# Performance work log

Measured on AMD Instinct MI355X. Metric: run time of the kernel, lower is better.

The kernel has to match this reference:

```python
import jax, jax.numpy as jnp
import numpy as np

EPS = 1e-6
KH = KW = 3  # square kernel the 5-point plus stencil unpacks into


def setup_inputs() -> dict:
    key = jax.random.key(0)
    k1, k2, k3 = jax.random.split(key, 3)
    bs, ci, co, H, W = 8, 256, 256, 128, 128
    x = jax.random.normal(k1, (bs, ci, H, W), dtype=jnp.float32)
    y = jax.random.normal(k2, (bs, ci), dtype=jnp.float32)
    # packed stencil weights (channels_out, channels_in, stencil_size)
    weights = jax.random.normal(k3, (co, ci, 5), dtype=jnp.float32) * 0.02
    # flat indices into the 3x3 kernel for stencil pts (0,1),(1,0),(1,1),(1,2),(2,1)
    stencil_index = jnp.array([1, 3, 4, 5, 7], dtype=jnp.int32)
    return {"x": x, "y": y, "weights": weights, "stencil_index": stencil_index}


def _modulated_lattice_conv(x, y, weights, stencil_index):
    bs, ci, H, W = x.shape
    co = weights.shape[0]
    # StyleGAN2-style modulation: w2 * (w1 + 1)  -> [bs, co, ci, S]
    w = weights[None, :, :, :] * (y[:, None, :, None] + 1.0)
    # demodulation: rsqrt of sum over (in, stencil) dims
    d = jax.lax.rsqrt(jnp.sum(w * w, axis=(2, 3), keepdims=True) + EPS)
    w = w * d
    # fold batch into output channels for groups=batch trick
    w = w.reshape(bs * co, ci, -1)
    # unpack non-square stencil into zero-padded square kernel (irregular scatter)
    full = jnp.zeros((bs * co, ci, KH * KW), dtype=w.dtype)
    full = full.at[:, :, stencil_index].set(w)
    kern = full.reshape(bs * co, ci, KH, KW)
    # grouped conv: input reshaped to (1, bs*ci, H, W), feature_group_count=bs
    out = jax.lax.conv_general_dilated(
        x.reshape(1, bs * ci, H, W), kern,
        window_strides=(1, 1), padding='SAME',
        feature_group_count=bs,
        dimension_numbers=('NCHW', 'OIHW', 'NCHW'))
    return out.reshape(bs, co, H, W)


def reference(x, y, weights, stencil_index):
    return _modulated_lattice_conv(x, y, weights, stencil_index)
```

## Files before the change

kernel.cpp:

```cpp
#include <hip/hip_runtime.h>


typedef short v8s __attribute__((ext_vector_type(8)));
typedef float v4f __attribute__((ext_vector_type(4)));
typedef int   v4i __attribute__((ext_vector_type(4)));

#define BS 8
#define CI 256
#define CO 256
#define HH 128
#define WW 128

#define WF_CK 10240
#define RSTR_B 5632
#define RSTR_I 1408
#define XBUF_I (6 * RSTR_I)
#define XBUF_B (6 * RSTR_B)

#define GLOAD_LDS16(g, l)                                                  \
    __builtin_amdgcn_global_load_lds(                                      \
        (__attribute__((address_space(1))) void*)(g),                      \
        (__attribute__((address_space(3))) void*)(l), 16, 0, 0)

__device__ __forceinline__ unsigned short f2bf(float f) {
    unsigned u = __builtin_bit_cast(unsigned, f);
    u += 0x7FFFu + ((u >> 16) & 1u);
    return (unsigned short)(u >> 16);
}

__global__ __launch_bounds__(256) void prep_kernel(const float* __restrict__ x,
                                                   const float* __restrict__ y,
                                                   const float* __restrict__ wgt,
                                                   short* __restrict__ wfrag,
                                                   unsigned int* __restrict__ xt) {
    __shared__ float tr[32 * 132];
    __shared__ float red[4];

    if (blockIdx.x < 2048) {
        const int bo = blockIdx.x;
        const int b = bo >> 8, o = bo & 255;
        const int ci = threadIdx.x;
        const float ym = y[b * CI + ci] + 1.0f;
        const float* wp = wgt + (o * CI + ci) * 5;
        float w[5];
        float s2 = 0.f;
        #pragma unroll
        for (int s = 0; s < 5; ++s) { w[s] = wp[s]; s2 += w[s] * w[s]; }
        float ss = ym * ym * s2;
        #pragma unroll
        for (int off = 32; off > 0; off >>= 1) ss += __shfl_down(ss, off);
        if ((threadIdx.x & 63) == 0) red[threadIdx.x >> 6] = ss;
        __syncthreads();
        const float tot = red[0] + red[1] + red[2] + red[3];
        const float scale = ym * rsqrtf(tot + 1e-6f);
        const int ot = o >> 6, mt = (o >> 4) & 3, m = o & 15;
        const int ck = ci >> 5, quad = (ci >> 3) & 3, j = ci & 7;
        size_t base = ((size_t)(b * 4 + ot) * 8 + ck) * WF_CK + quad * 128 + m * 8 + j;
        #pragma unroll
        for (int s = 0; s < 5; ++s)
            wfrag[base + (size_t)(s * 4 + mt) * 512] = (short)f2bf(w[s] * scale);
    } else {
        const int bid = blockIdx.x - 2048;
        const int b  = bid >> 10;
        const int ck = (bid >> 7) & 7;
        const int h  = bid & 127;
        const int tid = threadIdx.x;
        #pragma unroll
        for (int i = 0; i < 4; ++i) {
            int q  = tid + i * 256;
            int c  = q >> 5;
            int qp = q & 31;
            v4f v = *(const v4f*)&x[((size_t)(b * CI + ck * 32 + c) * HH + h) * WW
                                    + qp * 4];
            *(v4f*)&tr[c * 132 + qp * 4] = v;
        }
        __syncthreads();
        const int px = tid >> 1, half = tid & 1;
        unsigned pk[8];
        #pragma unroll
        for (int k = 0; k < 8; ++k) {
            float f0 = tr[(half * 16 + 2 * k)     * 132 + px];
            float f1 = tr[(half * 16 + 2 * k + 1) * 132 + px];
            pk[k] = (unsigned)f2bf(f0) | ((unsigned)f2bf(f1) << 16);
        }
        unsigned int* dst = xt + ((size_t)((b * 8 + ck) * 16384 + h * 128 + px)) * 16
                               + half * 8;
        *(v4i*)dst       = (v4i){(int)pk[0], (int)pk[1], (int)pk[2], (int)pk[3]};
        *(v4i*)(dst + 4) = (v4i){(int)pk[4], (int)pk[5], (int)pk[6], (int)pk[7]};
    }
}

__global__ __launch_bounds__(256) void wprep2_kernel(const float* __restrict__ y,
                                                     const float* __restrict__ wgt,
                                                     short* __restrict__ wfrag) {
    const int bo = blockIdx.x;
    const int b = bo >> 8, o = bo & 255;
    const int ci = threadIdx.x;
    const float ym = y[b * CI + ci] + 1.0f;
    const float* wp = wgt + (o * CI + ci) * 5;
    float w[5];
    float s2 = 0.f;
    #pragma unroll
    for (int s = 0; s < 5; ++s) { w[s] = wp[s]; s2 += w[s] * w[s]; }
    float ss = ym * ym * s2;
    #pragma unroll
    for (int off = 32; off > 0; off >>= 1) ss += __shfl_down(ss, off);
    __shared__ float red[4];
    if ((threadIdx.x & 63) == 0) red[threadIdx.x >> 6] = ss;
    __syncthreads();
    const float tot = red[0] + red[1] + red[2] + red[3];
    const float scale = ym * rsqrtf(tot + 1e-6f);
    const int ot = o >> 6, mt = (o >> 4) & 3, m = o & 15;
    const int ck = ci >> 5, quad = (ci >> 3) & 3, j = ci & 7;
    size_t base = ((size_t)(b * 4 + ot) * 8 + ck) * WF_CK + quad * 128 + m * 8 + j;
    #pragma unroll
    for (int s = 0; s < 5; ++s)
        wfrag[base + (size_t)(s * 4 + mt) * 512] = (short)f2bf(w[s] * scale);
}

__global__ __launch_bounds__(256, 2) void conv3_kernel(const char* __restrict__ xt,
                                                       const short* __restrict__ wfrag,
                                                       float* __restrict__ out) {
    const int b     = blockIdx.z;
    const int ot    = blockIdx.y;
    const int oBase = ot * 64;
    const int st    = blockIdx.x;
    const int r0    = (st >> 1) * 4;
    const int c0    = (st & 1) * 64;
    const bool left = (c0 == 0);

    const int tid  = threadIdx.x;
    const int wid  = tid >> 6;
    const int lane = tid & 63;
    const int l15  = lane & 15;
    const int quad = lane >> 4;

    __shared__ __align__(16) int xs[2 * XBUF_I];

    v4f acc[4][4];
    #pragma unroll
    for (int a = 0; a < 4; ++a)
        #pragma unroll
        for (int n = 0; n < 4; ++n) acc[a][n] = (v4f){0.f, 0.f, 0.f, 0.f};

    const v4i z4 = (v4i){0, 0, 0, 0};
    #pragma unroll
    for (int bb = 0; bb < 2; ++bb) {
        int* xb = xs + bb * XBUF_I;
        if (r0 == 0)
            for (int i = tid; i < 264; i += 256) *(v4i*)&xb[i * 4] = z4;
        if (r0 == HH - 4)
            for (int i = tid; i < 264; i += 256) *(v4i*)&xb[5 * RSTR_I + i * 4] = z4;
        if (left && tid < 24) *(v4i*)&xb[(tid >> 2) * RSTR_I + (tid & 3) * 4] = z4;
    }

    const int row = r0 + wid;
    const short* wfb = wfrag + (size_t)(b * 4 + ot) * 8 * WF_CK;
    const bool rz = (!left) && (l15 == 15);
    const int gstartB = left ? 0 : (c0 - 1) * 64;
    const int lshift  = left ? 64 : 0;

    auto stage = [&](int ckk, int bufsel) {
        const char* planep = xt + (((size_t)(b * 8 + ckk)) << 20);
        char* lbase = (char*)xs + bufsel * XBUF_B;
        #pragma unroll
        for (int rsel = 0; rsel < 2; ++rsel) {
            int rr = wid + rsel * 4;
            if (rr < 6) {
                bool skip = (r0 == 0 && rr == 0) || (r0 == HH - 4 && rr == 5);
                if (!skip) {
                    int gr = r0 - 1 + rr;
                    const char* gb = planep + (size_t)gr * 8192 + gstartB + lane * 16;
                    char* lb = lbase + rr * RSTR_B + lshift;
                    #pragma unroll
                    for (int t = 0; t < 5; ++t)
                        GLOAD_LDS16(gb + t * 1024, lb + t * 1024);
                }
            }
        }
    };

    stage(0, 0);
    __syncthreads();

    const int dh[5] = {-1, 0, 0, 0, 1};
    const int dw[5] = { 0,-1, 0, 1, 0};

    #pragma unroll 2
    for (int ck = 0; ck < 8; ++ck) {
        const short* wfc = wfb + (size_t)ck * WF_CK;
        const int* xb = xs + (ck & 1) * XBUF_I;

        v8s af[20];
        #pragma unroll
        for (int sm = 0; sm < 20; ++sm)
            af[sm] = *(const v8s*)(wfc + (size_t)(sm * 4 + quad) * 128 + l15 * 8);
        __builtin_amdgcn_sched_barrier(0);

        if (ck < 7) stage(ck + 1, (ck + 1) & 1);

        #pragma unroll
        for (int s = 0; s < 5; ++s) {
            const int xrow = wid + 1 + dh[s];
            const int xc0  = 1 + dw[s];
            #pragma unroll
            for (int nt = 0; nt < 4; ++nt) {
                v4i bi = *(const v4i*)&xb[xrow * RSTR_I + (nt * 16 + l15 + xc0) * 16
                                          + quad * 4];
                if (s == 3 && nt == 3) { if (rz) bi = z4; }
                v8s bfr = __builtin_bit_cast(v8s, bi);
                #pragma unroll
                for (int mt = 0; mt < 4; ++mt)
                    acc[mt][nt] = __builtin_amdgcn_mfma_f32_16x16x32_bf16(
                        af[s * 4 + mt], bfr, acc[mt][nt], 0, 0, 0);
            }
        }
        __syncthreads();
    }

    #pragma unroll
    for (int mt = 0; mt < 4; ++mt)
        #pragma unroll
        for (int nt = 0; nt < 4; ++nt)
            #pragma unroll
            for (int r = 0; r < 4; ++r) {
                int o = oBase + mt * 16 + quad * 4 + r;
                int c = c0 + nt * 16 + l15;
                out[((size_t)(b * CO + o) * HH + row) * WW + c] = acc[mt][nt][r];
            }
}

__global__ __launch_bounds__(256, 4) void conv_kernel(const float* __restrict__ x,
                                                      const short* __restrict__ wfrag,
                                                      float* __restrict__ out) {
    const int b     = blockIdx.z;
    const int ot    = blockIdx.y;
    const int oBase = ot * 64;
    const int st    = blockIdx.x;
    const int r0    = (st >> 1) * 4;
    const int c0    = (st & 1) * 64;
    const int tid  = threadIdx.x;
    const int wid  = tid >> 6;
    const int lane = tid & 63;
    const int l15  = lane & 15;
    const int quad = lane >> 4;
    #define PXS 20
    __shared__ __align__(16) int xs[6 * 66 * PXS];
    v4f acc[4][4];
    #pragma unroll
    for (int a = 0; a < 4; ++a)
        #pragma unroll
        for (int n = 0; n < 4; ++n) acc[a][n] = (v4f){0.f, 0.f, 0.f, 0.f};
    const int row = r0 + wid;
    const short* wfb = wfrag + (size_t)(b * 4 + ot) * 8 * WF_CK;
    const int dh[5] = {-1, 0, 0, 0, 1};
    const int dw[5] = { 0,-1, 0, 1, 0};
    for (int ck = 0; ck < 8; ++ck) {
        const int ic0 = ck * 32;
        #pragma unroll
        for (int t = 0; t < 6; ++t) {
            int idx = tid + t * 256;
            int cp  = idx & 15;
            int tmp = idx >> 4;
            int cq  = tmp & 15;
            int rr  = tmp >> 4;
            int gr  = r0 - 1 + rr;
            v4f a0 = (v4f){0.f, 0.f, 0.f, 0.f}, a1 = a0;
            if (gr >= 0 && gr < HH) {
                const float* xp = x + ((size_t)(b * CI + ic0 + cp * 2) * HH + gr) * WW
                                    + (c0 + cq * 4);
                a0 = *(const v4f*)xp;
                a1 = *(const v4f*)(xp + HH * WW);
            }
            int base = (rr * 66 + cq * 4 + 1) * PXS + cp;
            #pragma unroll
            for (int k = 0; k < 4; ++k)
                xs[base + k * PXS] =
                    (int)((unsigned)f2bf(a0[k]) | ((unsigned)f2bf(a1[k]) << 16));
        }
        if (tid < 192) {
            int cp   = tid & 15;
            int tmp  = tid >> 4;
            int side = (tmp >= 6) ? 1 : 0;
            int rr   = tmp - 6 * side;
            int gr   = r0 - 1 + rr;
            int gc   = side ? (c0 + 64) : (c0 - 1);
            float v0 = 0.f, v1 = 0.f;
            if (gr >= 0 && gr < HH && gc >= 0 && gc < WW) {
                const float* xp = x + ((size_t)(b * CI + ic0 + cp * 2) * HH + gr) * WW + gc;
                v0 = xp[0];
                v1 = xp[HH * WW];
            }
            int col = side ? 65 : 0;
            xs[(rr * 66 + col) * PXS + cp] =
                (int)((unsigned)f2bf(v0) | ((unsigned)f2bf(v1) << 16));
        }
        __syncthreads();
        const short* wfc = wfb + (size_t)ck * WF_CK;
        #pragma unroll
        for (int s = 0; s < 5; ++s) {
            const int xrow = wid + 1 + dh[s];
            const int xc0  = 1 + dw[s];
            v8s af[4];
            #pragma unroll
            for (int mt = 0; mt < 4; ++mt)
                af[mt] = *(const v8s*)(wfc + (size_t)((s * 4 + mt) * 4 + quad) * 128
                                           + l15 * 8);
            #pragma unroll
            for (int nt = 0; nt < 4; ++nt) {
                int px = xrow * 66 + nt * 16 + l15 + xc0;
                v4i bi = *(const v4i*)&xs[px * PXS + quad * 4];
                v8s bfr = __builtin_bit_cast(v8s, bi);
                #pragma unroll
                for (int mt = 0; mt < 4; ++mt)
                    acc[mt][nt] = __builtin_amdgcn_mfma_f32_16x16x32_bf16(
                        af[mt], bfr, acc[mt][nt], 0, 0, 0);
            }
        }
        __syncthreads();
    }
    #pragma unroll
    for (int mt = 0; mt < 4; ++mt)
        #pragma unroll
        for (int nt = 0; nt < 4; ++nt)
            #pragma unroll
            for (int r = 0; r < 4; ++r) {
                int o = oBase + mt * 16 + quad * 4 + r;
                int c = c0 + nt * 16 + l15;
                out[((size_t)(b * CO + o) * HH + row) * WW + c] = acc[mt][nt][r];
            }
}

__global__ __launch_bounds__(256) void demod_kernel(const float* __restrict__ y,
                                                    const float* __restrict__ wgt,
                                                    float* __restrict__ dbuf) {
    const int bo = blockIdx.x;
    const int b = bo >> 8, o = bo & 255;
    const int i = threadIdx.x;
    const float* wp = wgt + (o * CI + i) * 5;
    const float ym = y[b * CI + i] + 1.0f;
    float s2 = 0.f;
    #pragma unroll
    for (int s = 0; s < 5; ++s) { float w = wp[s]; s2 += w * w; }
    float val = ym * ym * s2;
    #pragma unroll
    for (int off = 32; off > 0; off >>= 1) val += __shfl_down(val, off);
    __shared__ float red[4];
    if ((threadIdx.x & 63) == 0) red[threadIdx.x >> 6] = val;
    __syncthreads();
    if (threadIdx.x == 0) dbuf[bo] = rsqrtf(red[0] + red[1] + red[2] + red[3] + 1e-6f);
}

__global__ __launch_bounds__(256) void conv_kernel_fb(const float* __restrict__ x,
                                                      const float* __restrict__ y,
                                                      const float* __restrict__ wgt,
                                                      const float* __restrict__ dbuf,
                                                      float* __restrict__ out) {
    const int b     = blockIdx.z;
    const int oBase = blockIdx.y * 64;
    const int st    = blockIdx.x;
    const int r0    = (st >> 1) * 4;
    const int c0    = (st & 1) * 64;
    const int tid  = threadIdx.x;
    const int wid  = tid >> 6;
    const int lane = tid & 63;
    const int l15  = lane & 15;
    const int quad = lane >> 4;
    __shared__ int   xs4[16 * 412];
    __shared__ short wlds[5 * 4 * 4 * 16 * 8];
    v4f acc[4][4];
    #pragma unroll
    for (int a = 0; a < 4; ++a)
        #pragma unroll
        for (int n = 0; n < 4; ++n) acc[a][n] = (v4f){0.f, 0.f, 0.f, 0.f};
    const int row = r0 + wid;
    for (int ic0 = 0; ic0 < CI; ic0 += 32) {
        for (int t = 0; t < 25; ++t) {
            int idx = tid + t * 256;
            if (idx < 6336) {
                int cp  = idx / 396;
                int rem = idx - cp * 396;
                int rr  = rem / 66;
                int cc  = rem - rr * 66;
                int gr  = r0 - 1 + rr;
                int gc  = c0 - 1 + cc;
                float v0 = 0.f, v1 = 0.f;
                if (gr >= 0 && gr < HH && gc >= 0 && gc < WW) {
                    const float* xp = x + ((size_t)(b * CI + ic0 + cp * 2) * HH + gr) * WW + gc;
                    v0 = xp[0];
                    v1 = xp[HH * WW];
                }
                xs4[cp * 412 + rr * 68 + cc] =
                    (int)((unsigned)f2bf(v0) | ((unsigned)f2bf(v1) << 16));
            }
        }
        #pragma unroll
        for (int p = 0; p < 8; ++p) {
            int pidx = tid + p * 256;
            int ol = pidx >> 5;
            int il = pidx & 31;
            int o  = oBase + ol;
            int ci = ic0 + il;
            float scale = (y[b * CI + ci] + 1.0f) * dbuf[b * CO + o];
            const float* wp = wgt + (o * CI + ci) * 5;
            int base = (((ol >> 4) * 4 + (il >> 3)) * 16 + (ol & 15)) * 8 + (il & 7);
            #pragma unroll
            for (int s = 0; s < 5; ++s)
                wlds[base + s * (4 * 4 * 16 * 8)] = (short)f2bf(wp[s] * scale);
        }
        __syncthreads();
        const int dh[5] = {-1, 0, 0, 0, 1};
        const int dw[5] = { 0,-1, 0, 1, 0};
        #pragma unroll
        for (int s = 0; s < 5; ++s) {
            int xrow = wid + 1 + dh[s];
            int xcb  = l15 + 1 + dw[s];
            v8s af[4];
            #pragma unroll
            for (int mt = 0; mt < 4; ++mt)
                af[mt] = *(const v8s*)&wlds[(((s * 4 + mt) * 4 + quad) * 16 + l15) * 8];
            #pragma unroll
            for (int nt = 0; nt < 4; ++nt) {
                v4i bi;
                #pragma unroll
                for (int p = 0; p < 4; ++p)
                    bi[p] = xs4[(quad * 4 + p) * 412 + xrow * 68 + nt * 16 + xcb];
                v8s bfr = __builtin_bit_cast(v8s, bi);
                #pragma unroll
                for (int mt = 0; mt < 4; ++mt)
                    acc[mt][nt] = __builtin_amdgcn_mfma_f32_16x16x32_bf16(
                        af[mt], bfr, acc[mt][nt], 0, 0, 0);
            }
        }
        __syncthreads();
    }
    #pragma unroll
    for (int mt = 0; mt < 4; ++mt)
        #pragma unroll
        for (int nt = 0; nt < 4; ++nt)
            #pragma unroll
            for (int r = 0; r < 4; ++r) {
                int o = oBase + mt * 16 + quad * 4 + r;
                int c = c0 + nt * 16 + l15;
                out[((size_t)(b * CO + o) * HH + row) * WW + c] = acc[mt][nt][r];
            }
}

extern "C" void kernel_launch(void* const* d_in, const int* in_sizes, int n_in,
                              void* d_out, int out_size, void* d_ws, size_t ws_size,
                              hipStream_t stream) {
    const float* x   = (const float*)d_in[0];
    const float* y   = (const float*)d_in[1];
    const float* wgt = (const float*)d_in[2];
    float* out = (float*)d_out;

    const size_t WF_BYTES = (size_t)BS * 4 * 8 * WF_CK * sizeof(short);
    const size_t XT_OFF   = WF_BYTES + 8192;
    const size_t XT_BYTES = (size_t)BS * 8 * 16384 * 64;
    const size_t NEED_FULL = XT_OFF + XT_BYTES + 1024;
    const size_t NEED_MID  = WF_BYTES + 8192;

    short* wfrag = (short*)d_ws;

    if (ws_size >= NEED_FULL) {
        unsigned int* xt = (unsigned int*)((char*)d_ws + XT_OFF);
        prep_kernel<<<dim3(2048 + BS * 8 * HH), dim3(256), 0, stream>>>(
            x, y, wgt, wfrag, xt);
        conv3_kernel<<<dim3(64, CO / 64, BS), dim3(256), 0, stream>>>(
            (const char*)xt, wfrag, out);
    } else if (ws_size >= NEED_MID) {
        wprep2_kernel<<<dim3(BS * CO), dim3(256), 0, stream>>>(y, wgt, wfrag);
        conv_kernel<<<dim3(64, CO / 64, BS), dim3(256), 0, stream>>>(x, wfrag, out);
    } else {
        float* dbuf = (float*)d_ws;
        demod_kernel<<<dim3(BS * CO), dim3(256), 0, stream>>>(y, wgt, dbuf);
        conv_kernel_fb<<<dim3(64, CO / 64, BS), dim3(256), 0, stream>>>(x, y, wgt, dbuf, out);
    }
}
```

Baseline: 312.3 us.

## Double rows per conv block and drop LDS double-buffering in conv3 kernel

Each conv3 block now covers 8 output rows instead of 4, so each wave computes two rows and reuses each weight fragment load across both rows. Halo rows are loaded 10 per 8 instead of 6 per 4, and the grid halves. The double-buffered prefetch is replaced by a single buffer with load-then-sync, which removes the overlap of global loads with MFMA work. Accumulators double to 128 floats per lane, which raises register pressure and may lower occupancy.

```diff
diff --git a/kernel.cpp b/kernel.cpp
--- a/kernel.cpp
+++ b/kernel.cpp
@@ -14,8 +14,6 @@
 #define WF_CK 10240
 #define RSTR_B 5632
 #define RSTR_I 1408
-#define XBUF_I (6 * RSTR_I)
-#define XBUF_B (6 * RSTR_B)
 
 #define GLOAD_LDS16(g, l)                                                  \
     __builtin_amdgcn_global_load_lds(                                      \
@@ -125,7 +123,7 @@
     const int ot    = blockIdx.y;
     const int oBase = ot * 64;
     const int st    = blockIdx.x;
-    const int r0    = (st >> 1) * 4;
+    const int r0    = (st >> 1) * 8;
     const int c0    = (st & 1) * 64;
     const bool left = (c0 == 0);
 
@@ -135,99 +133,92 @@
     const int l15  = lane & 15;
     const int quad = lane >> 4;
 
-    __shared__ __align__(16) int xs[2 * XBUF_I];
-
-    v4f acc[4][4];
-    #pragma unroll
-    for (int a = 0; a < 4; ++a)
-        #pragma unroll
-        for (int n = 0; n < 4; ++n) acc[a][n] = (v4f){0.f, 0.f, 0.f, 0.f};
+    __shared__ __align__(16) int xs[10 * RSTR_I];
+
+    v4f acc[2][4][4];
+    #pragma unroll
+    for (int r = 0; r < 2; ++r)
+        #pragma unroll
+        for (int a = 0; a < 4; ++a)
+            #pragma unroll
+            for (int n = 0; n < 4; ++n) acc[r][a][n] = (v4f){0.f, 0.f, 0.f, 0.f};
 
     const v4i z4 = (v4i){0, 0, 0, 0};
-    #pragma unroll
-    for (int bb = 0; bb < 2; ++bb) {
-        int* xb = xs + bb * XBUF_I;
-        if (r0 == 0)
-            for (int i = tid; i < 264; i += 256) *(v4i*)&xb[i * 4] = z4;
-        if (r0 == HH - 4)
-            for (int i = tid; i < 264; i += 256) *(v4i*)&xb[5 * RSTR_I + i * 4] = z4;
-        if (left && tid < 24) *(v4i*)&xb[(tid >> 2) * RSTR_I + (tid & 3) * 4] = z4;
-    }
-
-    const int row = r0 + wid;
+    if (r0 == 0)
+        for (int i = tid; i < 264; i += 256) *(v4i*)&xs[i * 4] = z4;
+    if (r0 == HH - 8)
+        for (int i = tid; i < 264; i += 256) *(v4i*)&xs[9 * RSTR_I + i * 4] = z4;
+    if (left && tid < 40) *(v4i*)&xs[(tid >> 2) * RSTR_I + (tid & 3) * 4] = z4;
+
     const short* wfb = wfrag + (size_t)(b * 4 + ot) * 8 * WF_CK;
     const bool rz = (!left) && (l15 == 15);
     const int gstartB = left ? 0 : (c0 - 1) * 64;
     const int lshift  = left ? 64 : 0;
 
-    auto stage = [&](int ckk, int bufsel) {
-        const char* planep = xt + (((size_t)(b * 8 + ckk)) << 20);
-        char* lbase = (char*)xs + bufsel * XBUF_B;
-        #pragma unroll
-        for (int rsel = 0; rsel < 2; ++rsel) {
+    const int dh[5] = {-1, 0, 0, 0, 1};
+    const int dw[5] = { 0,-1, 0, 1, 0};
+
+    for (int ck = 0; ck < 8; ++ck) {
+        const char* planep = xt + (((size_t)(b * 8 + ck)) << 20);
+        #pragma unroll
+        for (int rsel = 0; rsel < 3; ++rsel) {
             int rr = wid + rsel * 4;
-            if (rr < 6) {
-                bool skip = (r0 == 0 && rr == 0) || (r0 == HH - 4 && rr == 5);
+            if (rr < 10) {
+                bool skip = (r0 == 0 && rr == 0) || (r0 == HH - 8 && rr == 9);
                 if (!skip) {
                     int gr = r0 - 1 + rr;
                     const char* gb = planep + (size_t)gr * 8192 + gstartB + lane * 16;
-                    char* lb = lbase + rr * RSTR_B + lshift;
+                    char* lb = (char*)xs + rr * RSTR_B + lshift;
                     #pragma unroll
                     for (int t = 0; t < 5; ++t)
                         GLOAD_LDS16(gb + t * 1024, lb + t * 1024);
                 }
             }
         }
-    };
-
-    stage(0, 0);
-    __syncthreads();
-
-    const int dh[5] = {-1, 0, 0, 0, 1};
-    const int dw[5] = { 0,-1, 0, 1, 0};
-
-    #pragma unroll 2
-    for (int ck = 0; ck < 8; ++ck) {
+        __syncthreads();
+
         const short* wfc = wfb + (size_t)ck * WF_CK;
-        const int* xb = xs + (ck & 1) * XBUF_I;
-
-        v8s af[20];
-        #pragma unroll
-        for (int sm = 0; sm < 20; ++sm)
-            af[sm] = *(const v8s*)(wfc + (size_t)(sm * 4 + quad) * 128 + l15 * 8);
-        __builtin_amdgcn_sched_barrier(0);
-
-        if (ck < 7) stage(ck + 1, (ck + 1) & 1);
-
         #pragma unroll
         for (int s = 0; s < 5; ++s) {
-            const int xrow = wid + 1 + dh[s];
-            const int xc0  = 1 + dw[s];
-            #pragma unroll
-            for (int nt = 0; nt < 4; ++nt) {
-                v4i bi = *(const v4i*)&xb[xrow * RSTR_I + (nt * 16 + l15 + xc0) * 16
-                                          + quad * 4];
-                if (s == 3 && nt == 3) { if (rz) bi = z4; }
-                v8s bfr = __builtin_bit_cast(v8s, bi);
+            const int xc0 = 1 + dw[s];
+            v8s af[4];
+            #pragma unroll
+            for (int mt = 0; mt < 4; ++mt)
+                af[mt] = *(const v8s*)(wfc + (size_t)((s * 4 + mt) * 4 + quad) * 128
+                                           + l15 * 8);
+            #pragma unroll
+            for (int r = 0; r < 2; ++r) {
+                const int xrow = 2 * wid + r + 1 + dh[s];
                 #pragma unroll
-                for (int mt = 0; mt < 4; ++mt)
-                    acc[mt][nt] = __builtin_amdgcn_mfma_f32_16x16x32_bf16(
-                        af[s * 4 + mt], bfr, acc[mt][nt], 0, 0, 0);
-            }
-        }
-        __syncthreads();
-    }
-
-    #pragma unroll
-    for (int mt = 0; mt < 4; ++mt)
-        #pragma unroll
-        for (int nt = 0; nt < 4; ++nt)
-            #pragma unroll
-            for (int r = 0; r < 4; ++r) {
-                int o = oBase + mt * 16 + quad * 4 + r;
-                int c = c0 + nt * 16 + l15;
-                out[((size_t)(b * CO + o) * HH + row) * WW + c] = acc[mt][nt][r];
-            }
+                for (int nt = 0; nt < 4; ++nt) {
+                    v4i bi = *(const v4i*)&xs[xrow * RSTR_I
+                                              + (nt * 16 + l15 + xc0) * 16 + quad * 4];
+                    if (s == 3 && nt == 3) { if (rz) bi = z4; }
+                    v8s bfr = __builtin_bit_cast(v8s, bi);
+                    #pragma unroll
+                    for (int mt = 0; mt < 4; ++mt)
+                        acc[r][mt][nt] = __builtin_amdgcn_mfma_f32_16x16x32_bf16(
+                            af[mt], bfr, acc[r][mt][nt], 0, 0, 0);
+                }
+            }
+        }
+        __syncthreads();
+    }
+
+    #pragma unroll
+    for (int r = 0; r < 2; ++r) {
+        const int row = r0 + 2 * wid + r;
+        #pragma unroll
+        for (int mt = 0; mt < 4; ++mt)
+            #pragma unroll
+            for (int nt = 0; nt < 4; ++nt)
+                #pragma unroll
+                for (int rg = 0; rg < 4; ++rg) {
+                    int o = oBase + mt * 16 + quad * 4 + rg;
+                    int c = c0 + nt * 16 + l15;
+                    out[((size_t)(b * CO + o) * HH + row) * WW + c] = acc[r][mt][nt][rg];
+                }
+    }
 }
 
 __global__ __launch_bounds__(256, 4) void conv_kernel(const float* __restrict__ x,
@@ -466,7 +457,7 @@
         unsigned int* xt = (unsigned int*)((char*)d_ws + XT_OFF);
         prep_kernel<<<dim3(2048 + BS * 8 * HH), dim3(256), 0, stream>>>(
             x, y, wgt, wfrag, xt);
-        conv3_kernel<<<dim3(64, CO / 64, BS), dim3(256), 0, stream>>>(
+        conv3_kernel<<<dim3(32, CO / 64, BS), dim3(256), 0, stream>>>(
             (const char*)xt, wfrag, out);
     } else if (ws_size >= NEED_MID) {
         wprep2_kernel<<<dim3(BS * CO), dim3(256), 0, stream>>>(y, wgt, wfrag);
```

Result: no change. 314.0 us (+0.5%).

## Swizzle LDS tile layout and pipeline staging with explicit vmcnt waits

Applied to the files above, without the earlier changes.

Rewrites the input staging so every wave issues a uniform eight global-to-LDS loads, with row indices clamped instead of skipped. Boundary zero-padding moves out of LDS pre-zeroing and into register masks at MFMA operand load time. An XOR swizzle is applied to the LDS layout to reduce bank conflicts, and the read offsets are precomputed. Per-iteration __syncthreads is replaced by manual s_waitcnt vmcnt counters plus s_barrier, so weight loads and next-chunk staging overlap with compute. The hand-counted vmcnt values are fragile: they depend on exact load counts, and a miscount could cause a race.

```diff
diff --git a/kernel.cpp b/kernel.cpp
--- a/kernel.cpp
+++ b/kernel.cpp
@@ -143,71 +143,73 @@
         #pragma unroll
         for (int n = 0; n < 4; ++n) acc[a][n] = (v4f){0.f, 0.f, 0.f, 0.f};
 
-    const v4i z4 = (v4i){0, 0, 0, 0};
-    #pragma unroll
-    for (int bb = 0; bb < 2; ++bb) {
-        int* xb = xs + bb * XBUF_I;
-        if (r0 == 0)
-            for (int i = tid; i < 264; i += 256) *(v4i*)&xb[i * 4] = z4;
-        if (r0 == HH - 4)
-            for (int i = tid; i < 264; i += 256) *(v4i*)&xb[5 * RSTR_I + i * 4] = z4;
-        if (left && tid < 24) *(v4i*)&xb[(tid >> 2) * RSTR_I + (tid & 3) * 4] = z4;
-    }
-
     const int row = r0 + wid;
     const short* wfb = wfrag + (size_t)(b * 4 + ot) * 8 * WF_CK;
-    const bool rz = (!left) && (l15 == 15);
-    const int gstartB = left ? 0 : (c0 - 1) * 64;
-    const int lshift  = left ? 64 : 0;
+    const int gstartB = (c0 - 1) * 64;
+
+    const bool rzm  = (!left) && (l15 == 15);
+    const bool lzm  = left && (l15 == 0);
+    const bool topz = (r0 == 0)      && (wid == 0);
+    const bool botz = (r0 == HH - 4) && (wid == 3);
+    const v4i z4 = (v4i){0, 0, 0, 0};
+
+    const int dh[5] = {-1, 0, 0, 0, 1};
+    const int dw[5] = { 0,-1, 0, 1, 0};
+
+    int goff[8], loff[8];
+    #pragma unroll
+    for (int k = 0; k < 8; ++k) {
+        int q  = wid + 4 * k;
+        int qq = q < 30 ? q : q - 2;
+        int rr = qq / 5, t = qq - rr * 5;
+        int gr = r0 - 1 + rr;
+        gr = gr < 0 ? 0 : (gr > 127 ? 127 : gr);
+        int l  = t * 64 + lane;
+        int gx = l ^ ((l >> 3) & 7);
+        goff[k] = gr * 8192 + gstartB + gx * 16;
+        loff[k] = rr * RSTR_B + l * 16;
+    }
+
+    int boff[5][4];
+    #pragma unroll
+    for (int s = 0; s < 5; ++s) {
+        const int xrow = wid + 1 + dh[s];
+        const int xc0  = 1 + dw[s];
+        #pragma unroll
+        for (int nt = 0; nt < 4; ++nt) {
+            int slot = nt * 16 + l15 + xc0;
+            int gran = slot * 4 + quad;
+            int sg   = gran ^ ((gran >> 3) & 7);
+            boff[s][nt] = xrow * RSTR_I + sg * 4;
+        }
+    }
 
     auto stage = [&](int ckk, int bufsel) {
         const char* planep = xt + (((size_t)(b * 8 + ckk)) << 20);
         char* lbase = (char*)xs + bufsel * XBUF_B;
         #pragma unroll
-        for (int rsel = 0; rsel < 2; ++rsel) {
-            int rr = wid + rsel * 4;
-            if (rr < 6) {
-                bool skip = (r0 == 0 && rr == 0) || (r0 == HH - 4 && rr == 5);
-                if (!skip) {
-                    int gr = r0 - 1 + rr;
-                    const char* gb = planep + (size_t)gr * 8192 + gstartB + lane * 16;
-                    char* lb = lbase + rr * RSTR_B + lshift;
-                    #pragma unroll
-                    for (int t = 0; t < 5; ++t)
-                        GLOAD_LDS16(gb + t * 1024, lb + t * 1024);
-                }
-            }
-        }
+        for (int k = 0; k < 8; ++k)
+            GLOAD_LDS16(planep + goff[k], lbase + loff[k]);
     };
 
-    stage(0, 0);
-    __syncthreads();
-
-    const int dh[5] = {-1, 0, 0, 0, 1};
-    const int dw[5] = { 0,-1, 0, 1, 0};
-
-    #pragma unroll 2
-    for (int ck = 0; ck < 8; ++ck) {
+    v8s af[20];
+    auto load_af = [&](int ck) {
         const short* wfc = wfb + (size_t)ck * WF_CK;
-        const int* xb = xs + (ck & 1) * XBUF_I;
-
-        v8s af[20];
         #pragma unroll
         for (int sm = 0; sm < 20; ++sm)
             af[sm] = *(const v8s*)(wfc + (size_t)(sm * 4 + quad) * 128 + l15 * 8);
-        __builtin_amdgcn_sched_barrier(0);
-
-        if (ck < 7) stage(ck + 1, (ck + 1) & 1);
-
+    };
+
+    auto conv_step = [&](const int* xb) {
         #pragma unroll
         for (int s = 0; s < 5; ++s) {
-            const int xrow = wid + 1 + dh[s];
-            const int xc0  = 1 + dw[s];
             #pragma unroll
             for (int nt = 0; nt < 4; ++nt) {
-                v4i bi = *(const v4i*)&xb[xrow * RSTR_I + (nt * 16 + l15 + xc0) * 16
-                                          + quad * 4];
-                if (s == 3 && nt == 3) { if (rz) bi = z4; }
+                v4i bi = *(const v4i*)&xb[boff[s][nt]];
+                if (s == 0)            { if (topz) bi = z4; }
+                if (s == 4)            { if (botz) bi = z4; }
+                if (s == 1 && nt == 0) { if (lzm)  bi = z4; }
+                if (s == 3 && nt == 3) { if (rzm)  bi = z4; }
                 v8s bfr = __builtin_bit_cast(v8s, bi);
                 #pragma unroll
                 for (int mt = 0; mt < 4; ++mt)
@@ -215,8 +217,22 @@
                         af[s * 4 + mt], bfr, acc[mt][nt], 0, 0, 0);
             }
         }
-        __syncthreads();
-    }
+    };
+
+    stage(0, 0);
+    for (int ck = 0; ck < 7; ++ck) {
+        load_af(ck);
+        asm volatile("s_waitcnt vmcnt(20)" ::: "memory");
+        __builtin_amdgcn_s_barrier();
+        stage(ck + 1, (ck + 1) & 1);
+        asm volatile("s_waitcnt vmcnt(8)" ::: "memory");
+        conv_step(xs + (ck & 1) * XBUF_I);
+    }
+    load_af(7);
+    asm volatile("s_waitcnt vmcnt(20)" ::: "memory");
+    __builtin_amdgcn_s_barrier();
+    asm volatile("s_waitcnt vmcnt(0)" ::: "memory");
+    conv_step(xs + XBUF_I);
 
     #pragma unroll
     for (int mt = 0; mt < 4; ++mt)
```

After: 310.7 us. Within noise of the previous version (-0.5%).

## Drop double buffering in conv3 for higher occupancy; batch 4 rows per prep block

Applied to the files above, without the earlier changes.

The conv kernel replaces its double-buffered LDS staging and its up-front 20-fragment weight preload with a single buffer, loads 4 weight fragments per stencil point, and raises launch bounds to 4 blocks per CU. The aim is to cut LDS and register use so more waves can hide latency. In exchange, the overlap between global-to-LDS copies and MFMA work inside each block is lost. Separately, each prep block now transposes 4 rows instead of 1, which quarters the transpose grid and adds an extra barrier per row.

```diff
diff --git a/kernel.cpp b/kernel.cpp
--- a/kernel.cpp
+++ b/kernel.cpp
@@ -14,8 +14,6 @@
 #define WF_CK 10240
 #define RSTR_B 5632
 #define RSTR_I 1408
-#define XBUF_I (6 * RSTR_I)
-#define XBUF_B (6 * RSTR_B)
 
 #define GLOAD_LDS16(g, l)                                                  \
     __builtin_amdgcn_global_load_lds(                                      \
@@ -61,32 +59,37 @@
             wfrag[base + (size_t)(s * 4 + mt) * 512] = (short)f2bf(w[s] * scale);
     } else {
         const int bid = blockIdx.x - 2048;
-        const int b  = bid >> 10;
-        const int ck = (bid >> 7) & 7;
-        const int h  = bid & 127;
+        const int b  = bid >> 8;
+        const int ck = (bid >> 5) & 7;
+        const int h4 = bid & 31;
         const int tid = threadIdx.x;
         #pragma unroll
-        for (int i = 0; i < 4; ++i) {
-            int q  = tid + i * 256;
-            int c  = q >> 5;
-            int qp = q & 31;
-            v4f v = *(const v4f*)&x[((size_t)(b * CI + ck * 32 + c) * HH + h) * WW
-                                    + qp * 4];
-            *(v4f*)&tr[c * 132 + qp * 4] = v;
-        }
-        __syncthreads();
-        const int px = tid >> 1, half = tid & 1;
-        unsigned pk[8];
-        #pragma unroll
-        for (int k = 0; k < 8; ++k) {
-            float f0 = tr[(half * 16 + 2 * k)     * 132 + px];
-            float f1 = tr[(half * 16 + 2 * k + 1) * 132 + px];
-            pk[k] = (unsigned)f2bf(f0) | ((unsigned)f2bf(f1) << 16);
-        }
-        unsigned int* dst = xt + ((size_t)((b * 8 + ck) * 16384 + h * 128 + px)) * 16
-                               + half * 8;
-        *(v4i*)dst       = (v4i){(int)pk[0], (int)pk[1], (int)pk[2], (int)pk[3]};
-        *(v4i*)(dst + 4) = (v4i){(int)pk[4], (int)pk[5], (int)pk[6], (int)pk[7]};
+        for (int r = 0; r < 4; ++r) {
+            const int h = h4 * 4 + r;
+            #pragma unroll
+            for (int i = 0; i < 4; ++i) {
+                int q  = tid + i * 256;
+                int c  = q >> 5;
+                int qp = q & 31;
+                v4f v = *(const v4f*)&x[((size_t)(b * CI + ck * 32 + c) * HH + h) * WW
+                                        + qp * 4];
+                *(v4f*)&tr[c * 132 + qp * 4] = v;
+            }
+            __syncthreads();
+            const int px = tid >> 1, half = tid & 1;
+            unsigned pk[8];
+            #pragma unroll
+            for (int k = 0; k < 8; ++k) {
+                float f0 = tr[(half * 16 + 2 * k)     * 132 + px];
+                float f1 = tr[(half * 16 + 2 * k + 1) * 132 + px];
+                pk[k] = (unsigned)f2bf(f0) | ((unsigned)f2bf(f1) << 16);
+            }
+            unsigned int* dst = xt + ((size_t)((b * 8 + ck) * 16384 + h * 128 + px)) * 16
+                                   + half * 8;
+            *(v4i*)dst       = (v4i){(int)pk[0], (int)pk[1], (int)pk[2], (int)pk[3]};
+            *(v4i*)(dst + 4) = (v4i){(int)pk[4], (int)pk[5], (int)pk[6], (int)pk[7]};
+            __syncthreads();
+        }
     }
 }
 
@@ -118,7 +121,7 @@
         wfrag[base + (size_t)(s * 4 + mt) * 512] = (short)f2bf(w[s] * scale);
 }
 
-__global__ __launch_bounds__(256, 2) void conv3_kernel(const char* __restrict__ xt,
+__global__ __launch_bounds__(256, 4) void conv3_kernel(const char* __restrict__ xt,
                                                        const short* __restrict__ wfrag,
                                                        float* __restrict__ out) {
     const int b     = blockIdx.z;
@@ -135,7 +138,7 @@
     const int l15  = lane & 15;
     const int quad = lane >> 4;
 
-    __shared__ __align__(16) int xs[2 * XBUF_I];
+    __shared__ __align__(16) int xs[6 * RSTR_I];
 
     v4f acc[4][4];
     #pragma unroll
@@ -144,15 +147,11 @@
         for (int n = 0; n < 4; ++n) acc[a][n] = (v4f){0.f, 0.f, 0.f, 0.f};
 
     const v4i z4 = (v4i){0, 0, 0, 0};
-    #pragma unroll
-    for (int bb = 0; bb < 2; ++bb) {
-        int* xb = xs + bb * XBUF_I;
-        if (r0 == 0)
-            for (int i = tid; i < 264; i += 256) *(v4i*)&xb[i * 4] = z4;
-        if (r0 == HH - 4)
-            for (int i = tid; i < 264; i += 256) *(v4i*)&xb[5 * RSTR_I + i * 4] = z4;
-        if (left && tid < 24) *(v4i*)&xb[(tid >> 2) * RSTR_I + (tid & 3) * 4] = z4;
-    }
+    if (r0 == 0)
+        for (int i = tid; i < 264; i += 256) *(v4i*)&xs[i * 4] = z4;
+    if (r0 == HH - 4)
+        for (int i = tid; i < 264; i += 256) *(v4i*)&xs[5 * RSTR_I + i * 4] = z4;
+    if (left && tid < 24) *(v4i*)&xs[(tid >> 2) * RSTR_I + (tid & 3) * 4] = z4;
 
     const int row = r0 + wid;
     const short* wfb = wfrag + (size_t)(b * 4 + ot) * 8 * WF_CK;
@@ -160,9 +159,11 @@
     const int gstartB = left ? 0 : (c0 - 1) * 64;
     const int lshift  = left ? 64 : 0;
 
-    auto stage = [&](int ckk, int bufsel) {
-        const char* planep = xt + (((size_t)(b * 8 + ckk)) << 20);
-        char* lbase = (char*)xs + bufsel * XBUF_B;
+    const int dh[5] = {-1, 0, 0, 0, 1};
+    const int dw[5] = { 0,-1, 0, 1, 0};
+
+    for (int ck = 0; ck < 8; ++ck) {
+        const char* planep = xt + (((size_t)(b * 8 + ck)) << 20);
         #pragma unroll
         for (int rsel = 0; rsel < 2; ++rsel) {
             int rr = wid + rsel * 4;
@@ -171,48 +172,35 @@
                 if (!skip) {
                     int gr = r0 - 1 + rr;
                     const char* gb = planep + (size_t)gr * 8192 + gstartB + lane * 16;
-                    char* lb = lbase + rr * RSTR_B + lshift;
+                    char* lb = (char*)xs + rr * RSTR_B + lshift;
                     #pragma unroll
                     for (int t = 0; t < 5; ++t)
                         GLOAD_LDS16(gb + t * 1024, lb + t * 1024);
                 }
             }
         }
-    };
-
-    stage(0, 0);
-    __syncthreads();
-
-    const int dh[5] = {-1, 0, 0, 0, 1};
-    const int dw[5] = { 0,-1, 0, 1, 0};
-
-    #pragma unroll 2
-    for (int ck = 0; ck < 8; ++ck) {
+        __syncthreads();
+
         const short* wfc = wfb + (size_t)ck * WF_CK;
-        const int* xb = xs + (ck & 1) * XBUF_I;
-
-        v8s af[20];
-        #pragma unroll
-        for (int sm = 0; sm < 20; ++sm)
-            af[sm] = *(const v8s*)(wfc + (size_t)(sm * 4 + quad) * 128 + l15 * 8);
-        __builtin_amdgcn_sched_barrier(0);
-
-        if (ck < 7) stage(ck + 1, (ck + 1) & 1);
-
         #pragma unroll
         for (int s = 0; s < 5; ++s) {
             const int xrow = wid + 1 + dh[s];
             const int xc0  = 1 + dw[s];
+            v8s af[4];
+            #pragma unroll
+            for (int mt = 0; mt < 4; ++mt)
+                af[mt] = *(const v8s*)(wfc + (size_t)((s * 4 + mt) * 4 + quad) * 128
+                                           + l15 * 8);
             #pragma unroll
             for (int nt = 0; nt < 4; ++nt) {
-                v4i bi = *(const v4i*)&xb[xrow * RSTR_I + (nt * 16 + l15 + xc0) * 16
+                v4i bi = *(const v4i*)&xs[xrow * RSTR_I + (nt * 16 + l15 + xc0) * 16
                                           + quad * 4];
                 if (s == 3 && nt == 3) { if (rz) bi = z4; }
                 v8s bfr = __builtin_bit_cast(v8s, bi);
                 #pragma unroll
                 for (int mt = 0; mt < 4; ++mt)
                     acc[mt][nt] = __builtin_amdgcn_mfma_f32_16x16x32_bf16(
-                        af[s * 4 + mt], bfr, acc[mt][nt], 0, 0, 0);
+                        af[mt], bfr, acc[mt][nt], 0, 0, 0);
             }
         }
         __syncthreads();
@@ -464,7 +452,7 @@
 
     if (ws_size >= NEED_FULL) {
         unsigned int* xt = (unsigned int*)((char*)d_ws + XT_OFF);
-        prep_kernel<<<dim3(2048 + BS * 8 * HH), dim3(256), 0, stream>>>(
+        prep_kernel<<<dim3(2048 + BS * 8 * 32), dim3(256), 0, stream>>>(
             x, y, wgt, wfrag, xt);
         conv3_kernel<<<dim3(64, CO / 64, BS), dim3(256), 0, stream>>>(
             (const char*)xt, wfrag, out);
```

New measurement: 312.8 us. Within noise of the previous version (+0.2%).
